# Optimization experiments

Hardware: AMD Instinct MI355X
Metric: run time of the kernel (lower is better)

## Reference

```python
import jax, jax.numpy as jnp
import numpy as np

N, E = 100000, 1600000
IN_C, H, C = 256, 4, 64
NEG_SLOPE = 0.2


def setup_inputs() -> dict:
    key = jax.random.key(0)
    k1, k2, k3, k4, k5 = jax.random.split(key, 5)
    x = jax.random.normal(k1, (N, IN_C), dtype=jnp.float32)
    edge_index = jax.random.randint(k2, (2, E), 0, N, dtype=jnp.int64)
    # GATConv params: lin weight [IN_C, H*C], attention vectors [H, C], bias [C] (concat=False)
    W = jax.random.normal(k3, (IN_C, H * C), dtype=jnp.float32) / np.sqrt(IN_C)
    att_src = jax.random.normal(k4, (H, C), dtype=jnp.float32) / np.sqrt(C)
    att_dst = jax.random.normal(k5, (H, C), dtype=jnp.float32) / np.sqrt(C)
    bias = jnp.zeros((C,), dtype=jnp.float32)
    return {"x": x, "edge_index": edge_index, "W": W,
            "att_src": att_src, "att_dst": att_dst, "bias": bias}


def reference(x, edge_index, W, att_src, att_dst, bias):
    n = x.shape[0]
    # GATConv adds self-loops by default
    loops = jnp.arange(n, dtype=edge_index.dtype)
    src = jnp.concatenate([edge_index[0], loops])  # message source j
    dst = jnp.concatenate([edge_index[1], loops])  # message target i

    h = (x @ W).reshape(n, H, C)                       # [N,H,C]
    a_src = jnp.einsum('nhc,hc->nh', h, att_src)       # [N,H]
    a_dst = jnp.einsum('nhc,hc->nh', h, att_dst)       # [N,H]

    e = jax.nn.leaky_relu(a_src[src] + a_dst[dst], NEG_SLOPE)  # [E+N,H]
    m = jax.ops.segment_max(e, dst, num_segments=n)            # per-target max
    e = jnp.exp(e - m[dst])
    denom = jax.ops.segment_sum(e, dst, num_segments=n)
    alpha = e / (denom[dst] + 1e-16)                           # softmax over incoming edges

    out = jax.ops.segment_sum(alpha[:, :, None] * h[src], dst, num_segments=n)  # [N,H,C]
    return out.mean(axis=1) + bias  # concat=False -> mean over heads, [N,C]
```

## Files before the change

kernel.cpp:

```cpp
#include <hip/hip_runtime.h>

#define N_NODES 100000
#define N_EDGES 1600000
#define TOT (N_EDGES + N_NODES)
#define IN_CH 256
#define NHEAD 4
#define CH 64
#define HC 256
#define NEG_SLOPE 0.2f

typedef _Float16 half8 __attribute__((ext_vector_type(8)));
typedef _Float16 h2v __attribute__((ext_vector_type(2)));
typedef float f32x4 __attribute__((ext_vector_type(4)));
typedef unsigned short ushort_t;
typedef unsigned int uint_t;

static __device__ __forceinline__ ushort_t f2h(float f) {
  _Float16 h = (_Float16)f;
  return __builtin_bit_cast(ushort_t, h);
}

static __device__ __forceinline__ void gload_lds16(const char* g, char* l) {
  __builtin_amdgcn_global_load_lds(
      (const __attribute__((address_space(1))) unsigned int*)g,
      (__attribute__((address_space(3))) unsigned int*)l, 16, 0, 0);
}

__global__ __launch_bounds__(256) void conv_w(const float* __restrict__ W,
                                              uint4* __restrict__ Wt_arr) {
  int id = blockIdx.x * 256 + threadIdx.x;
  int lane = id & 63;
  int n = (id >> 6) & 15;
  int ks = id >> 10;
  int col = n * 16 + (lane & 15);
  int kbase = ks * 32 + (lane >> 4) * 8;
  ushort_t h[8];
#pragma unroll
  for (int j = 0; j < 8; ++j) h[j] = f2h(W[(size_t)(kbase + j) * HC + col]);
  uint4 u;
  u.x = (uint_t)h[0] | ((uint_t)h[1] << 16);
  u.y = (uint_t)h[2] | ((uint_t)h[3] << 16);
  u.z = (uint_t)h[4] | ((uint_t)h[5] << 16);
  u.w = (uint_t)h[6] | ((uint_t)h[7] << 16);
  Wt_arr[id] = u;
}

__global__ __launch_bounds__(256) void gemm_mfma(const float* __restrict__ X,
                                                 const uint4* __restrict__ Wt_arr,
                                                 const float* __restrict__ att_src,
                                                 const float* __restrict__ att_dst,
                                                 uint2* __restrict__ Hmp,
                                                 float* __restrict__ as_out,
                                                 float* __restrict__ ad_out, int M) {
  __shared__ uint4 Bs[2][1024];
  __shared__ __align__(16) float As[2][2048];
  const int tid = threadIdx.x;
  const int lane = tid & 63;
  const int wid = tid >> 6;
  const int l16 = lane & 15;
  const int lhi = lane >> 4;
  const int row0 = blockIdx.x * 64;

  const int arow = tid >> 3;
  const int aslot = tid & 7;
  int ga0 = row0 + arow;       if (ga0 >= M) ga0 = M - 1;
  int ga1 = row0 + arow + 32;  if (ga1 >= M) ga1 = M - 1;
  const int sslot = aslot ^ (arow & 7);
  const char* asrc0 = (const char*)X + (size_t)ga0 * 1024 + (sslot << 4);
  const char* asrc1 = (const char*)X + (size_t)ga1 * 1024 + (sslot << 4);
  char* adst0 = (char*)&As[0][0] + tid * 16;
  char* adst1 = (char*)&As[1][0] + tid * 16;

  const char* __restrict__ wsrc = (const char*)Wt_arr;
  char* bd0 = (char*)&Bs[0][0] + tid * 16;
  char* bd1 = (char*)&Bs[1][0] + tid * 16;

  const int frow = wid * 16 + l16;
  const int sw = frow & 7;
  const int fo0 = frow * 32 + (((2 * lhi + 0) ^ sw) << 2);
  const int fo1 = frow * 32 + (((2 * lhi + 1) ^ sw) << 2);

  gload_lds16(asrc0, adst0);
  gload_lds16(asrc1, adst0 + 4096);
  gload_lds16(wsrc + tid * 16,         bd0);
  gload_lds16(wsrc + 4096 + tid * 16,  bd0 + 4096);
  gload_lds16(wsrc + 8192 + tid * 16,  bd0 + 8192);
  gload_lds16(wsrc + 12288 + tid * 16, bd0 + 12288);

  f32x4 acc[16] = {};
  int cur = 0;

#pragma unroll
  for (int ks = 0; ks < 8; ++ks) {
    __syncthreads();

    if (ks < 7) {
      char* ad = (cur == 0) ? adst1 : adst0;
      gload_lds16(asrc0 + (ks + 1) * 128, ad);
      gload_lds16(asrc1 + (ks + 1) * 128, ad + 4096);
      char* bd = (cur == 0) ? bd1 : bd0;
      const char* s = wsrc + (ks + 1) * 16384 + tid * 16;
      gload_lds16(s,         bd);
      gload_lds16(s + 4096,  bd + 4096);
      gload_lds16(s + 8192,  bd + 8192);
      gload_lds16(s + 12288, bd + 12288);
    }

    const float* Ab = &As[cur][0];
    float4 f0 = *reinterpret_cast<const float4*>(Ab + fo0);
    float4 f1 = *reinterpret_cast<const float4*>(Ab + fo1);
    uint4 ua;
    ua.x = __builtin_bit_cast(uint_t, __builtin_amdgcn_cvt_pkrtz(f0.x, f0.y));
    ua.y = __builtin_bit_cast(uint_t, __builtin_amdgcn_cvt_pkrtz(f0.z, f0.w));
    ua.z = __builtin_bit_cast(uint_t, __builtin_amdgcn_cvt_pkrtz(f1.x, f1.y));
    ua.w = __builtin_bit_cast(uint_t, __builtin_amdgcn_cvt_pkrtz(f1.z, f1.w));
    half8 a = __builtin_bit_cast(half8, ua);

    const char* bbase = (const char*)&Bs[cur][0];
#pragma unroll
    for (int n = 0; n < 16; ++n) {
      half8 b = *reinterpret_cast<const half8*>(bbase + n * 1024 + lane * 16);
      acc[n] = __builtin_amdgcn_mfma_f32_16x16x32_f16(a, b, acc[n], 0, 0, 0);
    }
    cur ^= 1;
  }

  float attS[16], attD[16];
#pragma unroll
  for (int n = 0; n < 16; ++n) {
    attS[n] = att_src[n * 16 + l16];
    attD[n] = att_dst[n * 16 + l16];
  }

#pragma unroll
  for (int r = 0; r < 4; ++r) {
    int grow = row0 + wid * 16 + lhi * 4 + r;
    if (grow < M) {
#pragma unroll
      for (int n2 = 0; n2 < 4; ++n2) {
        uint_t pk01 = __builtin_bit_cast(uint_t,
            __builtin_amdgcn_cvt_pkrtz(acc[n2][r], acc[n2 + 4][r]));
        uint_t pk23 = __builtin_bit_cast(uint_t,
            __builtin_amdgcn_cvt_pkrtz(acc[n2 + 8][r], acc[n2 + 12][r]));
        Hmp[(size_t)grow * 64 + n2 * 16 + l16] = make_uint2(pk01, pk23);
      }
      float sv[4] = {0.f, 0.f, 0.f, 0.f}, dv[4] = {0.f, 0.f, 0.f, 0.f};
#pragma unroll
      for (int h = 0; h < 4; ++h)
#pragma unroll
        for (int j = 0; j < 4; ++j) {
          sv[h] += acc[h * 4 + j][r] * attS[h * 4 + j];
          dv[h] += acc[h * 4 + j][r] * attD[h * 4 + j];
        }
#pragma unroll
      for (int off = 1; off < 16; off <<= 1)
#pragma unroll
        for (int h = 0; h < 4; ++h) {
          sv[h] += __shfl_xor(sv[h], off, 16);
          dv[h] += __shfl_xor(dv[h], off, 16);
        }
      if (l16 == 0) {
#pragma unroll
        for (int h = 0; h < 4; ++h) {
          as_out[(size_t)grow * 4 + h] = sv[h];
          ad_out[(size_t)grow * 4 + h] = dv[h];
        }
      }
    }
  }
}

__global__ __launch_bounds__(256) void count_deg(const int* __restrict__ edst,
                                                 int* __restrict__ deg) {
  int t = blockIdx.x * 256 + threadIdx.x;
  if (t >= N_EDGES / 4) return;
  int4 d4 = reinterpret_cast<const int4*>(edst)[t];
  atomicAdd(&deg[d4.x], 1);
  atomicAdd(&deg[d4.y], 1);
  atomicAdd(&deg[d4.z], 1);
  atomicAdd(&deg[d4.w], 1);
}

__global__ __launch_bounds__(256) void scan1(const int* __restrict__ deg,
                                             int* __restrict__ rp,
                                             int* __restrict__ bsum) {
  __shared__ int sh[256];
  int t = threadIdx.x;
  int base = blockIdx.x * 1024 + t * 4;
  int v[4];
#pragma unroll
  for (int i = 0; i < 4; ++i) v[i] = (base + i < N_NODES) ? (deg[base + i] + 1) : 0;
  int tsum = v[0] + v[1] + v[2] + v[3];
  sh[t] = tsum;
  __syncthreads();
  for (int off = 1; off < 256; off <<= 1) {
    int x = (t >= off) ? sh[t - off] : 0;
    __syncthreads();
    sh[t] += x;
    __syncthreads();
  }
  if (t == 255) bsum[blockIdx.x] = sh[255];
  int run = sh[t] - tsum;
#pragma unroll
  for (int i = 0; i < 4; ++i) {
    if (base + i < N_NODES) rp[base + i] = run;
    run += v[i];
  }
}

#define NBLK1 ((N_NODES + 1023) / 1024)

__global__ __launch_bounds__(128) void scan2(const int* __restrict__ bsum,
                                             int* __restrict__ boff) {
  __shared__ int sh[128];
  int t = threadIdx.x;
  int own = (t < NBLK1) ? bsum[t] : 0;
  sh[t] = own;
  __syncthreads();
  for (int off = 1; off < 128; off <<= 1) {
    int x = (t >= off) ? sh[t - off] : 0;
    __syncthreads();
    sh[t] += x;
    __syncthreads();
  }
  boff[t] = sh[t] - own;
}

__global__ __launch_bounds__(256) void scan3(int* __restrict__ rp,
                                             const int* __restrict__ boff,
                                             int* __restrict__ cursor) {
  int idx = blockIdx.x * 256 + threadIdx.x;
  if (idx < N_NODES) {
    int v = rp[idx] + boff[idx >> 10];
    rp[idx] = v;
    cursor[idx] = v;
  }
  if (idx == 0) rp[N_NODES] = TOT;
}

__global__ __launch_bounds__(256) void scatter_edges(const int* __restrict__ esrc,
                                                     const int* __restrict__ edst,
                                                     const float* __restrict__ as_buf,
                                                     const float* __restrict__ ad_buf,
                                                     int* __restrict__ cursor,
                                                     uint4* __restrict__ erec) {
  int e = blockIdx.x * 256 + threadIdx.x;
  if (e >= TOT) return;
  int s, d;
  if (e < N_EDGES) { s = esrc[e]; d = edst[e]; }
  else { s = e - N_EDGES; d = s; }
  int p = atomicAdd(&cursor[d], 1);
  float4 a1 = *reinterpret_cast<const float4*>(as_buf + (size_t)s * NHEAD);
  float4 a2 = *reinterpret_cast<const float4*>(ad_buf + (size_t)d * NHEAD);
  float e0 = a1.x + a2.x; e0 = e0 > 0.f ? e0 : NEG_SLOPE * e0;
  float e1 = a1.y + a2.y; e1 = e1 > 0.f ? e1 : NEG_SLOPE * e1;
  float e2 = a1.z + a2.z; e2 = e2 > 0.f ? e2 : NEG_SLOPE * e2;
  float e3 = a1.w + a2.w; e3 = e3 > 0.f ? e3 : NEG_SLOPE * e3;
  float w0 = __expf(e0 - 4.f), w1 = __expf(e1 - 4.f);
  float w2 = __expf(e2 - 4.f), w3 = __expf(e3 - 4.f);
  uint_t pk01 = __builtin_bit_cast(uint_t, __builtin_amdgcn_cvt_pkrtz(w0, w1));
  uint_t pk23 = __builtin_bit_cast(uint_t, __builtin_amdgcn_cvt_pkrtz(w2, w3));
  erec[p] = make_uint4((uint_t)s, pk01, pk23, 0u);
}

__global__ __launch_bounds__(256) void aggregate(const int* __restrict__ rp,
                                                 const uint4* __restrict__ erec,
                                                 const uint2* __restrict__ Hp,
                                                 const float* __restrict__ bias,
                                                 float* __restrict__ out) {
  int n = blockIdx.x * 4 + (threadIdx.x >> 6);
  int lane = threadIdx.x & 63;
  if (n >= N_NODES) return;
  const int half = lane >> 5;
  const uint_t off_lane = (uint_t)(lane & 31) << 4;
  const char* __restrict__ Hb = (const char*)Hp;

  int beg = rp[n], end = rp[n + 1];
  const int last = end - 1;

  float acc[8] = {};
  float den[4] = {};

  int ia = beg + half;     if (ia > last) ia = last;
  int ib = beg + 2 + half; if (ib > last) ib = last;
  uint4 rec_a = erec[ia];
  uint4 rec_b = erec[ib];

  for (int j = beg; j < end; j += 4) {
    uint4 cur_a = rec_a;
    uint4 cur_b = rec_b;
    ia = j + 4 + half; if (ia > last) ia = last;
    ib = j + 6 + half; if (ib > last) ib = last;
    rec_a = erec[ia];
    rec_b = erec[ib];

    uint_t hoff_a = (cur_a.x << 9) | off_lane;
    uint_t hoff_b = (cur_b.x << 9) | off_lane;
    uint4 hva = *reinterpret_cast<const uint4*>(Hb + hoff_a);
    uint4 hvb = *reinterpret_cast<const uint4*>(Hb + hoff_b);

    bool act_a = (j + half) < end;
    bool act_b = (j + 2 + half) < end;
    uint_t wa01u = act_a ? cur_a.y : 0u;
    uint_t wa23u = act_a ? cur_a.z : 0u;
    uint_t wb01u = act_b ? cur_b.y : 0u;
    uint_t wb23u = act_b ? cur_b.z : 0u;

    h2v wa01 = __builtin_bit_cast(h2v, wa01u);
    h2v wa23 = __builtin_bit_cast(h2v, wa23u);
    h2v wb01 = __builtin_bit_cast(h2v, wb01u);
    h2v wb23 = __builtin_bit_cast(h2v, wb23u);

    h2v haa = __builtin_bit_cast(h2v, hva.x);
    h2v hab = __builtin_bit_cast(h2v, hva.y);
    h2v hac = __builtin_bit_cast(h2v, hva.z);
    h2v had = __builtin_bit_cast(h2v, hva.w);

    acc[0] += (float)wa01.x * (float)haa.x;
    acc[1] += (float)wa01.y * (float)haa.y;
    acc[2] += (float)wa23.x * (float)hab.x;
    acc[3] += (float)wa23.y * (float)hab.y;
    acc[4] += (float)wa01.x * (float)hac.x;
    acc[5] += (float)wa01.y * (float)hac.y;
    acc[6] += (float)wa23.x * (float)had.x;
    acc[7] += (float)wa23.y * (float)had.y;
    den[0] += (float)wa01.x;
    den[1] += (float)wa01.y;
    den[2] += (float)wa23.x;
    den[3] += (float)wa23.y;

    h2v hba = __builtin_bit_cast(h2v, hvb.x);
    h2v hbb = __builtin_bit_cast(h2v, hvb.y);
    h2v hbc = __builtin_bit_cast(h2v, hvb.z);
    h2v hbd = __builtin_bit_cast(h2v, hvb.w);

    acc[0] += (float)wb01.x * (float)hba.x;
    acc[1] += (float)wb01.y * (float)hba.y;
    acc[2] += (float)wb23.x * (float)hbb.x;
    acc[3] += (float)wb23.y * (float)hbb.y;
    acc[4] += (float)wb01.x * (float)hbc.x;
    acc[5] += (float)wb01.y * (float)hbc.y;
    acc[6] += (float)wb23.x * (float)hbd.x;
    acc[7] += (float)wb23.y * (float)hbd.y;
    den[0] += (float)wb01.x;
    den[1] += (float)wb01.y;
    den[2] += (float)wb23.x;
    den[3] += (float)wb23.y;
  }

#pragma unroll
  for (int k = 0; k < 8; ++k) acc[k] += __shfl_xor(acc[k], 32, 64);
#pragma unroll
  for (int k = 0; k < 4; ++k) den[k] += __shfl_xor(den[k], 32, 64);

  if (lane < 32) {
    float i0 = 1.f / (den[0] + 1e-30f);
    float i1 = 1.f / (den[1] + 1e-30f);
    float i2 = 1.f / (den[2] + 1e-30f);
    float i3 = 1.f / (den[3] + 1e-30f);
    float2 b2 = *reinterpret_cast<const float2*>(bias + 2 * lane);
    float rA = 0.25f * (acc[0] * i0 + acc[1] * i1 + acc[2] * i2 + acc[3] * i3) + b2.x;
    float rB = 0.25f * (acc[4] * i0 + acc[5] * i1 + acc[6] * i2 + acc[7] * i3) + b2.y;
    *reinterpret_cast<float2*>(out + (size_t)n * CH + 2 * lane) = make_float2(rA, rB);
  }
}

extern "C" void kernel_launch(void* const* d_in, const int* in_sizes, int n_in,
                              void* d_out, int out_size, void* d_ws, size_t ws_size,
                              hipStream_t stream) {
  const float* x       = (const float*)d_in[0];
  const int*   eidx    = (const int*)d_in[1];
  const float* W       = (const float*)d_in[2];
  const float* att_src = (const float*)d_in[3];
  const float* att_dst = (const float*)d_in[4];
  const float* bias    = (const float*)d_in[5];
  float* out = (float*)d_out;

  uint2* Hmp    = (uint2*)d_ws;
  uint4* erec   = (uint4*)(Hmp + (size_t)N_NODES * 64);
  float* as_buf = (float*)(erec + (size_t)TOT + 8);
  float* ad_buf = as_buf + (size_t)N_NODES * NHEAD;
  uint4* Wt_arr = (uint4*)(ad_buf + (size_t)N_NODES * NHEAD);
  int*   deg    = (int*)(Wt_arr + 8192);
  int*   rp     = deg + N_NODES;
  int*   bsum   = rp + N_NODES + 1;
  int*   boff   = bsum + 128;

  const int* esrc = eidx;
  const int* edst = eidx + N_EDGES;

  conv_w<<<32, 256, 0, stream>>>(W, Wt_arr);
  hipMemsetAsync(deg, 0, (size_t)N_NODES * sizeof(int), stream);
  count_deg<<<(N_EDGES / 4 + 255) / 256, 256, 0, stream>>>(edst, deg);

  dim3 ggrid((N_NODES + 63) / 64);
  gemm_mfma<<<ggrid, 256, 0, stream>>>(x, Wt_arr, att_src, att_dst, Hmp, as_buf, ad_buf,
                                       N_NODES);

  scan1<<<NBLK1, 256, 0, stream>>>(deg, rp, bsum);
  scan2<<<1, 128, 0, stream>>>(bsum, boff);
  scan3<<<(N_NODES + 255) / 256, 256, 0, stream>>>(rp, boff, deg );
  scatter_edges<<<(TOT + 255) / 256, 256, 0, stream>>>(esrc, edst, as_buf, ad_buf,
                                                       deg , erec);

  aggregate<<<(N_NODES + 3) / 4, 256, 0, stream>>>(rp, erec, Hmp, bias, out);
}
```

Measured before the change: 328.7 us.

## Fuse degree counting into GEMM launch and deepen aggregate edge prefetch

The degree-count kernel is merged into the GEMM launch as extra leading blocks, so the atomic histogram runs concurrently with the MFMA GEMM and one launch disappears. Separately, the aggregate loop now processes 8 edges per iteration with four outstanding record and feature loads per lane instead of two, raising memory-level parallelism for the gather. The fused grid puts the atomic-heavy blocks first, and the deeper unroll uses more registers, which could reduce occupancy and adds padded work for low-degree nodes.

```diff
diff --git a/kernel.cpp b/kernel.cpp
--- a/kernel.cpp
+++ b/kernel.cpp
@@ -8,6 +8,7 @@
 #define CH 64
 #define HC 256
 #define NEG_SLOPE 0.2f
+#define DEG_BLOCKS 391
 
 typedef _Float16 half8 __attribute__((ext_vector_type(8)));
 typedef _Float16 h2v __attribute__((ext_vector_type(2)));
@@ -51,15 +52,33 @@
                                                  const float* __restrict__ att_dst,
                                                  uint2* __restrict__ Hmp,
                                                  float* __restrict__ as_out,
-                                                 float* __restrict__ ad_out, int M) {
+                                                 float* __restrict__ ad_out,
+                                                 const int* __restrict__ edst,
+                                                 int* __restrict__ deg, int M) {
+  const int tid = threadIdx.x;
+
+  if (blockIdx.x < DEG_BLOCKS) {
+#pragma unroll
+    for (int i = 0; i < 4; ++i) {
+      int t = (blockIdx.x * 4 + i) * 256 + tid;
+      if (t < N_EDGES / 4) {
+        int4 d4 = reinterpret_cast<const int4*>(edst)[t];
+        atomicAdd(&deg[d4.x], 1);
+        atomicAdd(&deg[d4.y], 1);
+        atomicAdd(&deg[d4.z], 1);
+        atomicAdd(&deg[d4.w], 1);
+      }
+    }
+    return;
+  }
+
   __shared__ uint4 Bs[2][1024];
   __shared__ __align__(16) float As[2][2048];
-  const int tid = threadIdx.x;
   const int lane = tid & 63;
   const int wid = tid >> 6;
   const int l16 = lane & 15;
   const int lhi = lane >> 4;
-  const int row0 = blockIdx.x * 64;
+  const int row0 = (blockIdx.x - DEG_BLOCKS) * 64;
 
   const int arow = tid >> 3;
   const int aslot = tid & 7;
@@ -168,17 +187,6 @@
       }
     }
   }
-}
-
-__global__ __launch_bounds__(256) void count_deg(const int* __restrict__ edst,
-                                                 int* __restrict__ deg) {
-  int t = blockIdx.x * 256 + threadIdx.x;
-  if (t >= N_EDGES / 4) return;
-  int4 d4 = reinterpret_cast<const int4*>(edst)[t];
-  atomicAdd(&deg[d4.x], 1);
-  atomicAdd(&deg[d4.y], 1);
-  atomicAdd(&deg[d4.z], 1);
-  atomicAdd(&deg[d4.w], 1);
 }
 
 __global__ __launch_bounds__(256) void scan1(const int* __restrict__ deg,
@@ -263,6 +271,30 @@
   erec[p] = make_uint4((uint_t)s, pk01, pk23, 0u);
 }
 
+static __device__ __forceinline__ void accum_edge(uint4 cur, uint4 hv, bool act,
+                                                  float* acc, float* den) {
+  uint_t w01u = act ? cur.y : 0u;
+  uint_t w23u = act ? cur.z : 0u;
+  h2v w01 = __builtin_bit_cast(h2v, w01u);
+  h2v w23 = __builtin_bit_cast(h2v, w23u);
+  h2v ha = __builtin_bit_cast(h2v, hv.x);
+  h2v hb = __builtin_bit_cast(h2v, hv.y);
+  h2v hc = __builtin_bit_cast(h2v, hv.z);
+  h2v hd = __builtin_bit_cast(h2v, hv.w);
+  acc[0] += (float)w01.x * (float)ha.x;
+  acc[1] += (float)w01.y * (float)ha.y;
+  acc[2] += (float)w23.x * (float)hb.x;
+  acc[3] += (float)w23.y * (float)hb.y;
+  acc[4] += (float)w01.x * (float)hc.x;
+  acc[5] += (float)w01.y * (float)hc.y;
+  acc[6] += (float)w23.x * (float)hd.x;
+  acc[7] += (float)w23.y * (float)hd.y;
+  den[0] += (float)w01.x;
+  den[1] += (float)w01.y;
+  den[2] += (float)w23.x;
+  den[3] += (float)w23.y;
+}
+
 __global__ __launch_bounds__(256) void aggregate(const int* __restrict__ rp,
                                                  const uint4* __restrict__ erec,
                                                  const uint2* __restrict__ Hp,
@@ -281,71 +313,29 @@
   float acc[8] = {};
   float den[4] = {};
 
-  int ia = beg + half;     if (ia > last) ia = last;
-  int ib = beg + 2 + half; if (ib > last) ib = last;
-  uint4 rec_a = erec[ia];
-  uint4 rec_b = erec[ib];
-
-  for (int j = beg; j < end; j += 4) {
-    uint4 cur_a = rec_a;
-    uint4 cur_b = rec_b;
-    ia = j + 4 + half; if (ia > last) ia = last;
-    ib = j + 6 + half; if (ib > last) ib = last;
-    rec_a = erec[ia];
-    rec_b = erec[ib];
-
-    uint_t hoff_a = (cur_a.x << 9) | off_lane;
-    uint_t hoff_b = (cur_b.x << 9) | off_lane;
-    uint4 hva = *reinterpret_cast<const uint4*>(Hb + hoff_a);
-    uint4 hvb = *reinterpret_cast<const uint4*>(Hb + hoff_b);
-
-    bool act_a = (j + half) < end;
-    bool act_b = (j + 2 + half) < end;
-    uint_t wa01u = act_a ? cur_a.y : 0u;
-    uint_t wa23u = act_a ? cur_a.z : 0u;
-    uint_t wb01u = act_b ? cur_b.y : 0u;
-    uint_t wb23u = act_b ? cur_b.z : 0u;
-
-    h2v wa01 = __builtin_bit_cast(h2v, wa01u);
-    h2v wa23 = __builtin_bit_cast(h2v, wa23u);
-    h2v wb01 = __builtin_bit_cast(h2v, wb01u);
-    h2v wb23 = __builtin_bit_cast(h2v, wb23u);
-
-    h2v haa = __builtin_bit_cast(h2v, hva.x);
-    h2v hab = __builtin_bit_cast(h2v, hva.y);
-    h2v hac = __builtin_bit_cast(h2v, hva.z);
-    h2v had = __builtin_bit_cast(h2v, hva.w);
-
-    acc[0] += (float)wa01.x * (float)haa.x;
-    acc[1] += (float)wa01.y * (float)haa.y;
-    acc[2] += (float)wa23.x * (float)hab.x;
-    acc[3] += (float)wa23.y * (float)hab.y;
-    acc[4] += (float)wa01.x * (float)hac.x;
-    acc[5] += (float)wa01.y * (float)hac.y;
-    acc[6] += (float)wa23.x * (float)had.x;
-    acc[7] += (float)wa23.y * (float)had.y;
-    den[0] += (float)wa01.x;
-    den[1] += (float)wa01.y;
-    den[2] += (float)wa23.x;
-    den[3] += (float)wa23.y;
-
-    h2v hba = __builtin_bit_cast(h2v, hvb.x);
-    h2v hbb = __builtin_bit_cast(h2v, hvb.y);
-    h2v hbc = __builtin_bit_cast(h2v, hvb.z);
-    h2v hbd = __builtin_bit_cast(h2v, hvb.w);
-
-    acc[0] += (float)wb01.x * (float)hba.x;
-    acc[1] += (float)wb01.y * (float)hba.y;
-    acc[2] += (float)wb23.x * (float)hbb.x;
-    acc[3] += (float)wb23.y * (float)hbb.y;
-    acc[4] += (float)wb01.x * (float)hbc.x;
-    acc[5] += (float)wb01.y * (float)hbc.y;
-    acc[6] += (float)wb23.x * (float)hbd.x;
-    acc[7] += (float)wb23.y * (float)hbd.y;
-    den[0] += (float)wb01.x;
-    den[1] += (float)wb01.y;
-    den[2] += (float)wb23.x;
-    den[3] += (float)wb23.y;
+  int i0 = beg + half;     if (i0 > last) i0 = last;
+  int i1 = beg + 2 + half; if (i1 > last) i1 = last;
+  int i2 = beg + 4 + half; if (i2 > last) i2 = last;
+  int i3 = beg + 6 + half; if (i3 > last) i3 = last;
+  uint4 r0 = erec[i0], r1 = erec[i1], r2 = erec[i2], r3 = erec[i3];
+
+  for (int j = beg; j < end; j += 8) {
+    uint4 c0 = r0, c1 = r1, c2 = r2, c3 = r3;
+    i0 = j + 8 + half;  if (i0 > last) i0 = last;
+    i1 = j + 10 + half; if (i1 > last) i1 = last;
+    i2 = j + 12 + half; if (i2 > last) i2 = last;
+    i3 = j + 14 + half; if (i3 > last) i3 = last;
+    r0 = erec[i0]; r1 = erec[i1]; r2 = erec[i2]; r3 = erec[i3];
+
+    uint4 h0 = *reinterpret_cast<const uint4*>(Hb + ((c0.x << 9) | off_lane));
+    uint4 h1 = *reinterpret_cast<const uint4*>(Hb + ((c1.x << 9) | off_lane));
+    uint4 h2 = *reinterpret_cast<const uint4*>(Hb + ((c2.x << 9) | off_lane));
+    uint4 h3 = *reinterpret_cast<const uint4*>(Hb + ((c3.x << 9) | off_lane));
+
+    accum_edge(c0, h0, (j + half) < end, acc, den);
+    accum_edge(c1, h1, (j + 2 + half) < end, acc, den);
+    accum_edge(c2, h2, (j + 4 + half) < end, acc, den);
+    accum_edge(c3, h3, (j + 6 + half) < end, acc, den);
   }
 
 #pragma unroll
@@ -354,13 +344,13 @@
   for (int k = 0; k < 4; ++k) den[k] += __shfl_xor(den[k], 32, 64);
 
   if (lane < 32) {
-    float i0 = 1.f / (den[0] + 1e-30f);
-    float i1 = 1.f / (den[1] + 1e-30f);
-    float i2 = 1.f / (den[2] + 1e-30f);
-    float i3 = 1.f / (den[3] + 1e-30f);
+    float i0v = 1.f / (den[0] + 1e-30f);
+    float i1v = 1.f / (den[1] + 1e-30f);
+    float i2v = 1.f / (den[2] + 1e-30f);
+    float i3v = 1.f / (den[3] + 1e-30f);
     float2 b2 = *reinterpret_cast<const float2*>(bias + 2 * lane);
-    float rA = 0.25f * (acc[0] * i0 + acc[1] * i1 + acc[2] * i2 + acc[3] * i3) + b2.x;
-    float rB = 0.25f * (acc[4] * i0 + acc[5] * i1 + acc[6] * i2 + acc[7] * i3) + b2.y;
+    float rA = 0.25f * (acc[0] * i0v + acc[1] * i1v + acc[2] * i2v + acc[3] * i3v) + b2.x;
+    float rB = 0.25f * (acc[4] * i0v + acc[5] * i1v + acc[6] * i2v + acc[7] * i3v) + b2.y;
     *reinterpret_cast<float2*>(out + (size_t)n * CH + 2 * lane) = make_float2(rA, rB);
   }
 }
@@ -391,11 +381,10 @@
 
   conv_w<<<32, 256, 0, stream>>>(W, Wt_arr);
   hipMemsetAsync(deg, 0, (size_t)N_NODES * sizeof(int), stream);
-  count_deg<<<(N_EDGES / 4 + 255) / 256, 256, 0, stream>>>(edst, deg);
-
-  dim3 ggrid((N_NODES + 63) / 64);
+
+  dim3 ggrid(DEG_BLOCKS + (N_NODES + 63) / 64);
   gemm_mfma<<<ggrid, 256, 0, stream>>>(x, Wt_arr, att_src, att_dst, Hmp, as_buf, ad_buf,
-                                       N_NODES);
+                                       edst, deg, N_NODES);
 
   scan1<<<NBLK1, 256, 0, stream>>>(deg, rp, bsum);
   scan2<<<1, 128, 0, stream>>>(bsum, boff);
```

New measurement: 316.0 us. -3.8%, faster.
